# Kernel optimization log

Measured on AMD Instinct MI355X. Metric: run time of the kernel, lower is better.

The kernel has to match this reference:

```python
import jax, jax.numpy as jnp
import numpy as np

TEMPERATURE = 0.5
NEG_FILL = -1e9


def setup_inputs() -> dict:
    key = jax.random.key(0)
    k1, k2 = jax.random.split(key)
    B, D = 4096, 256
    z1 = jax.random.normal(k1, (B, D), dtype=jnp.float32)
    z2 = jax.random.normal(k2, (B, D), dtype=jnp.float32)
    return {"z1": z1, "z2": z2}


def reference(z1, z2):
    z = jnp.concatenate([z1, z2], axis=0)           # [n, d], n = 2B
    n = z.shape[0]
    half = n // 2
    sim = jnp.matmul(z, z.T) / TEMPERATURE          # [n, n]
    eye = jnp.eye(n, dtype=bool)
    sim = jnp.where(eye, NEG_FILL, sim)
    # targets: positive pair is the other view of the same sample
    idx = jnp.arange(n)
    targets = jnp.where(idx < half, idx + half, idx - half)
    logp = jax.nn.log_softmax(sim, axis=-1)         # stable softmax CE
    loss = -jnp.mean(jnp.take_along_axis(logp, targets[:, None], axis=1))
    return loss
```

## Files before the change

kernel.cpp:

```cpp
#include <hip/hip_runtime.h>

#define NROWS 8192
#define HALF  4096
#define DIM   256
#define JS    16
#define JRANGE (NROWS / JS)
#define JTILES (JRANGE / 16)
#define IPB   256
#define IPW   64

typedef short bf16x8 __attribute__((ext_vector_type(8)));
typedef float f32x4  __attribute__((ext_vector_type(4)));

__device__ __forceinline__ unsigned short f2bf(float f) {
    unsigned int u = __float_as_uint(f);
    u += 0x7FFFu + ((u >> 16) & 1u);
    return (unsigned short)(u >> 16);
}

__global__ void k_prep(const float* __restrict__ z1, const float* __restrict__ z2,
                       unsigned short* __restrict__ zb, float* __restrict__ pos,
                       float* __restrict__ out) {
    if (blockIdx.x == 0 && threadIdx.x == 0) *out = 0.0f;
    int w = threadIdx.x >> 6, lane = threadIdx.x & 63;
    int row = blockIdx.x * 4 + w;
    float4 a = *(const float4*)(z1 + (size_t)row * DIM + lane * 4);
    float4 b = *(const float4*)(z2 + (size_t)row * DIM + lane * 4);

    uint2 pa, pb;
    pa.x = (unsigned int)f2bf(a.x) | ((unsigned int)f2bf(a.y) << 16);
    pa.y = (unsigned int)f2bf(a.z) | ((unsigned int)f2bf(a.w) << 16);
    pb.x = (unsigned int)f2bf(b.x) | ((unsigned int)f2bf(b.y) << 16);
    pb.y = (unsigned int)f2bf(b.z) | ((unsigned int)f2bf(b.w) << 16);
    *(uint2*)(zb + (size_t)row * DIM + lane * 4)          = pa;
    *(uint2*)(zb + (size_t)(row + HALF) * DIM + lane * 4) = pb;

    float d = a.x * b.x + a.y * b.y + a.z * b.z + a.w * b.w;
    #pragma unroll
    for (int k = 32; k; k >>= 1) d += __shfl_xor(d, k);
    if (lane == 0) pos[row] = 2.0f * d;
}

__global__ __launch_bounds__(256, 2)
void k_main(const unsigned short* __restrict__ zb, float2* __restrict__ part) {
    __shared__ __align__(16) char lds[2][8192];
    char* ldsflat = &lds[0][0];

    const int tid  = threadIdx.x;
    const int w    = tid >> 6;
    const int lane = tid & 63;
    const int col  = lane & 15;
    const int kg   = lane >> 4;
    const int ib   = blockIdx.x & 31;
    const int js   = blockIdx.x >> 5;
    const int iw   = ib * IPB + w * IPW;
    const int jb0  = js * JRANGE;
    const int swz  = (lane & 7) << 4;

    const uint4* gz = (const uint4*)zb;

    bf16x8 bf[4][8];
    #pragma unroll
    for (int p = 0; p < 8; ++p) {
        size_t gbase = (size_t)(ib * IPB + p * 32) * 32;
        #pragma unroll
        for (int k = 0; k < 4; ++k) {
            int e  = tid + k * 256;
            uint4 v = gz[gbase + e];
            int lo = e * 16;
            int r  = lo >> 9;
            *(uint4*)(ldsflat + (lo ^ ((r & 7) << 4))) = v;
        }
        __syncthreads();
        if ((p >> 1) == w) {
            #pragma unroll
            for (int h = 0; h < 2; ++h) {
                const char* tb = ldsflat + h * 8192;
                #pragma unroll
                for (int kk = 0; kk < 8; ++kk)
                    bf[(p & 1) * 2 + h][kk] =
                        *(const bf16x8*)(tb + col * 512 + (((kk << 6) | (kg << 4)) ^ swz));
            }
        }
        __syncthreads();
    }

    float m[4], l[4];
    #pragma unroll
    for (int is = 0; is < 4; ++is) { m[is] = -1e30f; l[is] = 0.0f; }

    const int rbase = col * 512;
    const int dr    = col - kg * 4;

    {
        int jb = jb0;
        uint4 s0 = gz[jb * 32 + tid];
        uint4 s1 = gz[jb * 32 + 256 + tid];
        int lo0 = tid * 16;        int r0 = lo0 >> 9; int ph0 = lo0 ^ ((r0 & 7) << 4);
        int lo1 = 4096 + tid * 16; int r1 = lo1 >> 9; int ph1 = lo1 ^ ((r1 & 7) << 4);
        *(uint4*)(ldsflat + ph0) = s0;
        *(uint4*)(ldsflat + ph1) = s1;
    }
    __syncthreads();

    int cur = 0;
    for (int t = 0; t < JTILES; ++t) {
        const int jb = jb0 + t * 16;
        uint4 n0, n1;
        const bool more = (t + 1 < JTILES);
        if (more) {
            int jn = jb + 16;
            n0 = gz[jn * 32 + tid];
            n1 = gz[jn * 32 + 256 + tid];
        }

        bf16x8 af[8];
        const char* base = lds[cur];
        #pragma unroll
        for (int kk = 0; kk < 8; ++kk) {
            int inrow = (kk << 6) | (kg << 4);
            af[kk] = *(const bf16x8*)(base + rbase + (inrow ^ swz));
        }

        #pragma unroll
        for (int is = 0; is < 4; ++is) {
            f32x4 acc = {0.f, 0.f, 0.f, 0.f};
            #pragma unroll
            for (int kk = 0; kk < 8; ++kk)
                acc = __builtin_amdgcn_mfma_f32_16x16x32_bf16(af[kk], bf[is][kk], acc, 0, 0, 0);

            if (jb == iw + is * 16) {
                #pragma unroll
                for (int r = 0; r < 4; ++r)
                    if (dr == r) acc[r] = -1e30f;
            }
            float t0 = fmaxf(fmaxf(acc[0], acc[1]), fmaxf(acc[2], acc[3]));
            float mn = fmaxf(m[is], t0 * 2.0f);
            float s  = __expf(fmaf(acc[0], 2.0f, -mn)) + __expf(fmaf(acc[1], 2.0f, -mn))
                     + __expf(fmaf(acc[2], 2.0f, -mn)) + __expf(fmaf(acc[3], 2.0f, -mn));
            l[is] = l[is] * __expf(m[is] - mn) + s;
            m[is] = mn;
        }

        if (more) {
            char* dstb = lds[cur ^ 1];
            int lo0 = tid * 16;        int r0 = lo0 >> 9; int ph0 = lo0 ^ ((r0 & 7) << 4);
            int lo1 = 4096 + tid * 16; int r1 = lo1 >> 9; int ph1 = lo1 ^ ((r1 & 7) << 4);
            *(uint4*)(dstb + ph0) = n0;
            *(uint4*)(dstb + ph1) = n1;
        }
        __syncthreads();
        cur ^= 1;
    }

    #pragma unroll
    for (int is = 0; is < 4; ++is) {
        float mm = m[is], ll = l[is];
        #pragma unroll
        for (int msk = 16; msk <= 32; msk <<= 1) {
            float mo  = __shfl_xor(mm, msk);
            float lo_ = __shfl_xor(ll, msk);
            float mn  = fmaxf(mm, mo);
            ll = ll * __expf(mm - mn) + lo_ * __expf(mo - mn);
            mm = mn;
        }
        if (kg == 0) {
            int i = iw + is * 16 + col;
            part[i * JS + js] = make_float2(mm, ll);
        }
    }
}

__global__ void k_final(const float2* __restrict__ part, const float* __restrict__ pos,
                        float* __restrict__ out) {
    int tid = threadIdx.x;
    int i = blockIdx.x * 256 + tid;
    const float2* p = part + (size_t)i * JS;
    float2 v[JS];
    float M = -3e30f;
    #pragma unroll
    for (int s = 0; s < JS; ++s) { v[s] = p[s]; M = fmaxf(M, v[s].x); }
    float L = 0.0f;
    #pragma unroll
    for (int s = 0; s < JS; ++s) L += v[s].y * __expf(v[s].x - M);
    float loss = M + __logf(L) - pos[i & (HALF - 1)];

    #pragma unroll
    for (int k = 32; k; k >>= 1) loss += __shfl_down(loss, k);
    __shared__ float ps[4];
    int w = tid >> 6, lane = tid & 63;
    if (lane == 0) ps[w] = loss;
    __syncthreads();
    if (tid == 0) atomicAdd(out, (ps[0] + ps[1] + ps[2] + ps[3]) * (1.0f / (float)NROWS));
}

extern "C" void kernel_launch(void* const* d_in, const int* in_sizes, int n_in,
                              void* d_out, int out_size, void* d_ws, size_t ws_size,
                              hipStream_t stream) {
    const float* z1 = (const float*)d_in[0];
    const float* z2 = (const float*)d_in[1];
    float* out = (float*)d_out;

    char* ws = (char*)d_ws;
    unsigned short* zb = (unsigned short*)ws;
    float* pos  = (float*)(ws + 4u * 1024u * 1024u);
    float2* part = (float2*)(ws + 4u * 1024u * 1024u + 65536u);

    k_prep <<<1024, 256, 0, stream>>>(z1, z2, zb, pos, out);
    k_main <<<512,  256, 0, stream>>>(zb, part);
    k_final<<<32,   256, 0, stream>>>(part, pos, out);
}
```

Baseline: 106.4 us.

## Use direct global-to-LDS loads with four-buffer pipeline and lazy softmax rescale

Replaces register-staged global loads with global_load_lds direct-to-LDS copies, swizzling the source addresses so the loads still fill the XOR-swizzled layout. The j-tile loop moves from double to four buffers, processing two tiles per barrier. The 1/temperature scale is folded into bf16 inputs (times sqrt2) so the mfma output no longer needs doubling. The online softmax only rescales when any lane sees a new max. This raises LDS use to 32KB per block and adds precision risk from rounding the pre-scaled bf16 values.

```diff
diff --git a/kernel.cpp b/kernel.cpp
--- a/kernel.cpp
+++ b/kernel.cpp
@@ -4,13 +4,17 @@
 #define HALF  4096
 #define DIM   256
 #define JS    16
-#define JRANGE (NROWS / JS)
-#define JTILES (JRANGE / 16)
+#define JRANGE 512
+#define JTILES 32
 #define IPB   256
 #define IPW   64
 
 typedef short bf16x8 __attribute__((ext_vector_type(8)));
 typedef float f32x4  __attribute__((ext_vector_type(4)));
+
+#define GLOAD16(g, l) __builtin_amdgcn_global_load_lds( \
+    (const __attribute__((address_space(1))) unsigned int*)(g), \
+    (__attribute__((address_space(3))) unsigned int*)(l), 16, 0, 0)
 
 __device__ __forceinline__ unsigned short f2bf(float f) {
     unsigned int u = __float_as_uint(f);
@@ -22,16 +26,17 @@
                        unsigned short* __restrict__ zb, float* __restrict__ pos,
                        float* __restrict__ out) {
     if (blockIdx.x == 0 && threadIdx.x == 0) *out = 0.0f;
+    const float R2 = 1.41421356237309515f;
     int w = threadIdx.x >> 6, lane = threadIdx.x & 63;
     int row = blockIdx.x * 4 + w;
     float4 a = *(const float4*)(z1 + (size_t)row * DIM + lane * 4);
     float4 b = *(const float4*)(z2 + (size_t)row * DIM + lane * 4);
 
     uint2 pa, pb;
-    pa.x = (unsigned int)f2bf(a.x) | ((unsigned int)f2bf(a.y) << 16);
-    pa.y = (unsigned int)f2bf(a.z) | ((unsigned int)f2bf(a.w) << 16);
-    pb.x = (unsigned int)f2bf(b.x) | ((unsigned int)f2bf(b.y) << 16);
-    pb.y = (unsigned int)f2bf(b.z) | ((unsigned int)f2bf(b.w) << 16);
+    pa.x = (unsigned int)f2bf(a.x*R2) | ((unsigned int)f2bf(a.y*R2) << 16);
+    pa.y = (unsigned int)f2bf(a.z*R2) | ((unsigned int)f2bf(a.w*R2) << 16);
+    pb.x = (unsigned int)f2bf(b.x*R2) | ((unsigned int)f2bf(b.y*R2) << 16);
+    pb.y = (unsigned int)f2bf(b.z*R2) | ((unsigned int)f2bf(b.w*R2) << 16);
     *(uint2*)(zb + (size_t)row * DIM + lane * 4)          = pa;
     *(uint2*)(zb + (size_t)(row + HALF) * DIM + lane * 4) = pb;
 
@@ -43,7 +48,7 @@
 
 __global__ __launch_bounds__(256, 2)
 void k_main(const unsigned short* __restrict__ zb, float2* __restrict__ part) {
-    __shared__ __align__(16) char lds[2][8192];
+    __shared__ __align__(16) char lds[4][8192];
     char* ldsflat = &lds[0][0];
 
     const int tid  = threadIdx.x;
@@ -56,101 +61,101 @@
     const int iw   = ib * IPB + w * IPW;
     const int jb0  = js * JRANGE;
     const int swz  = (lane & 7) << 4;
-
-    const uint4* gz = (const uint4*)zb;
+    const int dr   = col - kg * 4;
+
+    const char* zbb = (const char*)zb;
+
+    const int jp0 = w * 1024 + lane * 16;
+    const int jp1 = 4096 + jp0;
+    const int jg0 = jp0 ^ (((jp0 >> 9) & 7) << 4);
+    const int jg1 = jp1 ^ (((jp1 >> 9) & 7) << 4);
 
     bf16x8 bf[4][8];
-    #pragma unroll
-    for (int p = 0; p < 8; ++p) {
-        size_t gbase = (size_t)(ib * IPB + p * 32) * 32;
+    {
+        int igo[4];
         #pragma unroll
         for (int k = 0; k < 4; ++k) {
-            int e  = tid + k * 256;
-            uint4 v = gz[gbase + e];
-            int lo = e * 16;
-            int r  = lo >> 9;
-            *(uint4*)(ldsflat + (lo ^ ((r & 7) << 4))) = v;
-        }
+            int p = k * 4096 + w * 1024 + lane * 16;
+            igo[k] = p ^ (((p >> 9) & 7) << 4);
+        }
+        #pragma unroll
+        for (int p = 0; p < 8; ++p) {
+            const char* gib = zbb + (size_t)(ib * IPB + p * 32) * 512;
+            #pragma unroll
+            for (int k = 0; k < 4; ++k)
+                GLOAD16(gib + igo[k], ldsflat + k * 4096 + w * 1024);
+            __syncthreads();
+            if ((p >> 1) == w) {
+                #pragma unroll
+                for (int h = 0; h < 2; ++h) {
+                    const char* tb = ldsflat + h * 8192;
+                    #pragma unroll
+                    for (int kk = 0; kk < 8; ++kk)
+                        bf[(p & 1) * 2 + h][kk] =
+                            *(const bf16x8*)(tb + col * 512 + (((kk << 6) | (kg << 4)) ^ swz));
+                }
+            }
+            __syncthreads();
+        }
+    }
+
+    float m[4], l[4];
+    #pragma unroll
+    for (int is = 0; is < 4; ++is) { m[is] = -1e30f; l[is] = 0.0f; }
+
+    const char* ap = ldsflat + col * 512;
+    int aoff[8];
+    #pragma unroll
+    for (int kk = 0; kk < 8; ++kk) aoff[kk] = ((kk << 6) | (kg << 4)) ^ swz;
+
+    const int dt = (iw - jb0) >> 4;
+    const char* jbase = zbb + (size_t)jb0 * 512;
+
+#define JSTAGE(T, B) do { \
+    GLOAD16(jbase + (size_t)(T) * 8192 + jg0, ldsflat + (B) * 8192 + w * 1024); \
+    GLOAD16(jbase + (size_t)(T) * 8192 + jg1, ldsflat + (B) * 8192 + 4096 + w * 1024); \
+} while (0)
+
+#define COMPUTE_TILE(B, T) do { \
+    bf16x8 af[8]; \
+    _Pragma("unroll") \
+    for (int kk = 0; kk < 8; ++kk) \
+        af[kk] = *(const bf16x8*)(ap + aoff[kk] + (B) * 8192); \
+    const int dd = (T) - dt; \
+    _Pragma("unroll") \
+    for (int is = 0; is < 4; ++is) { \
+        f32x4 acc = {0.f, 0.f, 0.f, 0.f}; \
+        _Pragma("unroll") \
+        for (int kk = 0; kk < 8; ++kk) \
+            acc = __builtin_amdgcn_mfma_f32_16x16x32_bf16(af[kk], bf[is][kk], acc, 0, 0, 0); \
+        if (dd == is) { \
+            _Pragma("unroll") \
+            for (int r = 0; r < 4; ++r) if (dr == r) acc[r] = -1e30f; \
+        } \
+        float t0 = fmaxf(fmaxf(acc[0], acc[1]), fmaxf(acc[2], acc[3])); \
+        if (__any(t0 > m[is])) {                  \
+            float mn = fmaxf(m[is], t0); \
+            l[is] *= __expf(m[is] - mn); \
+            m[is] = mn; \
+        } \
+        l[is] += __expf(acc[0] - m[is]) + __expf(acc[1] - m[is]) \
+               + __expf(acc[2] - m[is]) + __expf(acc[3] - m[is]); \
+    } \
+} while (0)
+
+    JSTAGE(0, 0); JSTAGE(1, 1);
+    __syncthreads();
+
+    for (int u = 0; u < 8; ++u) {
+        const int t = u * 4;
+        JSTAGE(t + 2, 2); JSTAGE(t + 3, 3);
+        COMPUTE_TILE(0, t);
+        COMPUTE_TILE(1, t + 1);
         __syncthreads();
-        if ((p >> 1) == w) {
-            #pragma unroll
-            for (int h = 0; h < 2; ++h) {
-                const char* tb = ldsflat + h * 8192;
-                #pragma unroll
-                for (int kk = 0; kk < 8; ++kk)
-                    bf[(p & 1) * 2 + h][kk] =
-                        *(const bf16x8*)(tb + col * 512 + (((kk << 6) | (kg << 4)) ^ swz));
-            }
-        }
+        if (u < 7) { JSTAGE(t + 4, 0); JSTAGE(t + 5, 1); }
+        COMPUTE_TILE(2, t + 2);
+        COMPUTE_TILE(3, t + 3);
         __syncthreads();
-    }
-
-    float m[4], l[4];
-    #pragma unroll
-    for (int is = 0; is < 4; ++is) { m[is] = -1e30f; l[is] = 0.0f; }
-
-    const int rbase = col * 512;
-    const int dr    = col - kg * 4;
-
-    {
-        int jb = jb0;
-        uint4 s0 = gz[jb * 32 + tid];
-        uint4 s1 = gz[jb * 32 + 256 + tid];
-        int lo0 = tid * 16;        int r0 = lo0 >> 9; int ph0 = lo0 ^ ((r0 & 7) << 4);
-        int lo1 = 4096 + tid * 16; int r1 = lo1 >> 9; int ph1 = lo1 ^ ((r1 & 7) << 4);
-        *(uint4*)(ldsflat + ph0) = s0;
-        *(uint4*)(ldsflat + ph1) = s1;
-    }
-    __syncthreads();
-
-    int cur = 0;
-    for (int t = 0; t < JTILES; ++t) {
-        const int jb = jb0 + t * 16;
-        uint4 n0, n1;
-        const bool more = (t + 1 < JTILES);
-        if (more) {
-            int jn = jb + 16;
-            n0 = gz[jn * 32 + tid];
-            n1 = gz[jn * 32 + 256 + tid];
-        }
-
-        bf16x8 af[8];
-        const char* base = lds[cur];
-        #pragma unroll
-        for (int kk = 0; kk < 8; ++kk) {
-            int inrow = (kk << 6) | (kg << 4);
-            af[kk] = *(const bf16x8*)(base + rbase + (inrow ^ swz));
-        }
-
-        #pragma unroll
-        for (int is = 0; is < 4; ++is) {
-            f32x4 acc = {0.f, 0.f, 0.f, 0.f};
-            #pragma unroll
-            for (int kk = 0; kk < 8; ++kk)
-                acc = __builtin_amdgcn_mfma_f32_16x16x32_bf16(af[kk], bf[is][kk], acc, 0, 0, 0);
-
-            if (jb == iw + is * 16) {
-                #pragma unroll
-                for (int r = 0; r < 4; ++r)
-                    if (dr == r) acc[r] = -1e30f;
-            }
-            float t0 = fmaxf(fmaxf(acc[0], acc[1]), fmaxf(acc[2], acc[3]));
-            float mn = fmaxf(m[is], t0 * 2.0f);
-            float s  = __expf(fmaf(acc[0], 2.0f, -mn)) + __expf(fmaf(acc[1], 2.0f, -mn))
-                     + __expf(fmaf(acc[2], 2.0f, -mn)) + __expf(fmaf(acc[3], 2.0f, -mn));
-            l[is] = l[is] * __expf(m[is] - mn) + s;
-            m[is] = mn;
-        }
-
-        if (more) {
-            char* dstb = lds[cur ^ 1];
-            int lo0 = tid * 16;        int r0 = lo0 >> 9; int ph0 = lo0 ^ ((r0 & 7) << 4);
-            int lo1 = 4096 + tid * 16; int r1 = lo1 >> 9; int ph1 = lo1 ^ ((r1 & 7) << 4);
-            *(uint4*)(dstb + ph0) = n0;
-            *(uint4*)(dstb + ph1) = n1;
-        }
-        __syncthreads();
-        cur ^= 1;
     }
 
     #pragma unroll
@@ -169,6 +174,8 @@
             part[i * JS + js] = make_float2(mm, ll);
         }
     }
+#undef JSTAGE
+#undef COMPUTE_TILE
 }
 
 __global__ void k_final(const float2* __restrict__ part, const float* __restrict__ pos,
```

New measurement: 101.8 us. 4.3% less time.
